# Kernel optimization log

Hardware: AMD Instinct MI355X
Metric: run time of the kernel (lower is better)

Reference implementation:

```python
import jax, jax.numpy as jnp
import numpy as np

B, T, D, H, L, V = 16, 1024, 512, 8, 6, 96
HS = D // H
FF = 4 * D


def setup_inputs() -> dict:
    key = jax.random.key(0)
    ks = jax.random.split(key, 16)
    n = lambda k, shape: jax.random.normal(k, shape, jnp.float32) * 0.02
    return {
        "idx": jax.random.randint(ks[0], (B, T), 0, V),
        "targets": jax.random.randint(ks[1], (B, T), 0, V),
        "tok_emb": n(ks[2], (V, D)),
        "pos_emb": n(ks[3], (T, D)),
        "Wq": n(ks[4], (L, H, D, HS)),
        "Wk": n(ks[5], (L, H, D, HS)),
        "Wv": n(ks[6], (L, H, D, HS)),
        "Wproj": n(ks[7], (L, D, D)),
        "bproj": jnp.zeros((L, D), jnp.float32),
        "W1": n(ks[8], (L, D, FF)),
        "b1": jnp.zeros((L, FF), jnp.float32),
        "W2": n(ks[9], (L, FF, D)),
        "b2": jnp.zeros((L, D), jnp.float32),
        "ln1_s": jnp.ones((L, D), jnp.float32),
        "ln1_b": jnp.zeros((L, D), jnp.float32),
        "ln2_s": jnp.ones((L, D), jnp.float32),
        "ln2_b": jnp.zeros((L, D), jnp.float32),
        "lnf_s": jnp.ones((D,), jnp.float32),
        "lnf_b": jnp.zeros((D,), jnp.float32),
        "Wout": n(ks[10], (D, V)),
        "bout": jnp.zeros((V,), jnp.float32),
    }


def _ln(x, s, b, eps=1e-5):
    m = x.mean(-1, keepdims=True)
    v = ((x - m) ** 2).mean(-1, keepdims=True)
    return (x - m) * jax.lax.rsqrt(v + eps) * s + b


def reference(idx, targets, tok_emb, pos_emb, Wq, Wk, Wv, Wproj, bproj,
              W1, b1, W2, b2, ln1_s, ln1_b, ln2_s, ln2_b, lnf_s, lnf_b,
              Wout, bout):
    x = tok_emb[idx] + pos_emb[:T]  # [B,T,D]
    causal = jnp.tril(jnp.ones((T, T), jnp.bool_))
    scale = D ** (-0.5)  # NOTE: source scales by full channel dim, not head_size
    for l in range(L):
        h = _ln(x, ln1_s[l], ln1_b[l])
        q = jnp.einsum("btd,hdk->bhtk", h, Wq[l])
        k = jnp.einsum("btd,hdk->bhtk", h, Wk[l])
        v = jnp.einsum("btd,hdk->bhtk", h, Wv[l])
        att = jnp.einsum("bhtk,bhsk->bhts", q, k) * scale
        att = jnp.where(causal, att, -jnp.inf)
        att = jax.nn.softmax(att, axis=-1)
        o = jnp.einsum("bhts,bhsk->bhtk", att, v)
        o = o.transpose(0, 2, 1, 3).reshape(B, T, D)  # concat heads
        x = x + (o @ Wproj[l] + bproj[l])
        h2 = _ln(x, ln2_s[l], ln2_b[l])
        x = x + (jnp.maximum(h2 @ W1[l] + b1[l], 0.0) @ W2[l] + b2[l])
    x = _ln(x, lnf_s, lnf_b)
    logits = (x @ Wout + bout).reshape(B * T, V)
    logp = jax.nn.log_softmax(logits, axis=-1)
    loss = -logp[jnp.arange(B * T), targets.reshape(-1)].mean()
    return logits, loss
```

## Files before the change

kernel.cpp:

```cpp
#include <hip/hip_runtime.h>

#define B_  16
#define T_  1024
#define D_  512
#define H_  8
#define L_  6
#define V_  96
#define HS_ 64
#define FF_ 2048
#define BT_ (B_*T_)
#define QKS 1024

typedef __attribute__((ext_vector_type(8))) short bf16x8;
typedef __attribute__((ext_vector_type(4))) float f32x4;

typedef __attribute__((address_space(3))) unsigned int lds_u32_t;
typedef const __attribute__((address_space(1))) unsigned int glb_u32_t;

__device__ __forceinline__ void gload16(const unsigned short* g, unsigned short* l) {
  __builtin_amdgcn_global_load_lds((glb_u32_t*)g, (lds_u32_t*)l, 16, 0, 0);
}

__device__ __forceinline__ unsigned short f2b(float f) {
  unsigned u = __float_as_uint(f);
  unsigned r = (u + 0x7FFFu + ((u >> 16) & 1u)) >> 16;
  return (unsigned short)r;
}

__global__ void zero_kernel(float* p) { p[0] = 0.f; }

__global__ __launch_bounds__(128) void embed_kernel(const int* __restrict__ idx,
    const float* __restrict__ tok, const float* __restrict__ pos, float* __restrict__ x) {
  int bt = blockIdx.x;
  int t  = bt & (T_ - 1);
  int id = idx[bt];
  if (id < 0) id = 0; if (id > V_ - 1) id = V_ - 1;
  int d  = threadIdx.x * 4;
  float4 tv = *(const float4*)(tok + (size_t)id * D_ + d);
  float4 pv = *(const float4*)(pos + (size_t)t  * D_ + d);
  float4 o = {tv.x + pv.x, tv.y + pv.y, tv.z + pv.z, tv.w + pv.w};
  *(float4*)(x + (size_t)bt * D_ + d) = o;
}

__global__ __launch_bounds__(256) void transpose_cvt(const float* __restrict__ src,
    unsigned short* __restrict__ dst, int R, int C, long sstride, long dstride,
    int zper, long zouter) {
  __shared__ float t[32][33];
  const float* s = src + (size_t)blockIdx.z * sstride;
  unsigned short* d = dst + (size_t)(blockIdx.z / zper) * zouter
                          + (size_t)(blockIdx.z % zper) * dstride;
  int r0 = blockIdx.y * 32, c0 = blockIdx.x * 32;
  int tr = threadIdx.x >> 5, tc = threadIdx.x & 31;
#pragma unroll
  for (int i = 0; i < 4; ++i)
    t[tr + i * 8][tc] = s[(size_t)(r0 + tr + i * 8) * C + c0 + tc];
  __syncthreads();
#pragma unroll
  for (int i = 0; i < 4; ++i)
    d[(size_t)(c0 + tr + i * 8) * R + r0 + tc] = f2b(t[tc][tr + i * 8]);
}

template<bool BF16OUT>
__global__ __launch_bounds__(256) void ln_kernel(const float* __restrict__ x,
    const float* __restrict__ s, const float* __restrict__ b, void* __restrict__ outv) {
  int wave = threadIdx.x >> 6;
  int lane = threadIdx.x & 63;
  int r = blockIdx.x * 4 + wave;
  const float* xr = x + (size_t)r * D_;
  float vals[8];
  float sum = 0.f;
#pragma unroll
  for (int j = 0; j < 8; ++j) { vals[j] = xr[j * 64 + lane]; sum += vals[j]; }
#pragma unroll
  for (int o = 32; o > 0; o >>= 1) sum += __shfl_xor(sum, o, 64);
  float mean = sum * (1.f / D_);
  float vs = 0.f;
#pragma unroll
  for (int j = 0; j < 8; ++j) { float d = vals[j] - mean; vs += d * d; }
#pragma unroll
  for (int o = 32; o > 0; o >>= 1) vs += __shfl_xor(vs, o, 64);
  float rstd = rsqrtf(vs * (1.f / D_) + 1e-5f);
#pragma unroll
  for (int j = 0; j < 8; ++j) {
    int c = j * 64 + lane;
    float v = (vals[j] - mean) * rstd * s[c] + b[c];
    if (BF16OUT) ((unsigned short*)outv)[(size_t)r * D_ + c] = f2b(v);
    else         ((float*)outv)[(size_t)r * D_ + c] = v;
  }
}

#define BK 32
template<bool ACC, bool RELU, bool BIAS, int OUTMODE, int MT, int NT>
__global__ __launch_bounds__(256) void mfma_gemm(
    const unsigned short* __restrict__ A,
    const unsigned short* __restrict__ Bt,
    const float* __restrict__ bias,
    void* __restrict__ Cv, void* __restrict__ Cv2,
    int K, int ldc) {
  constexpr int NI = (MT == 128) ? 4 : (NT == 128 ? 2 : 1);
  constexpr int WN = (MT == 128) ? 64 : (NT == 128 ? 32 : 16);
  __shared__ unsigned short Al[2][MT * BK];
  __shared__ unsigned short Bl[2][NT * BK];
  const int nwg = gridDim.x * gridDim.y;
  const int flat = blockIdx.x + gridDim.x * blockIdx.y;
  const int swz = (flat & 7) * (nwg >> 3) + (flat >> 3);
  const int bx = swz / gridDim.y;
  const int by = swz % gridDim.y;
  const int m0 = bx * MT, n0 = by * NT;
  const int tid = threadIdx.x;
  const int lane = tid & 63, wave = tid >> 6;
  const int wy = (MT == 128) ? (wave >> 1) : 0;
  const int wx = (MT == 128) ? (wave & 1) : wave;
  const int l15 = lane & 15, quad = lane >> 4;

  const int sbase = wave * 1024;
  const int soff  = sbase + lane * 16;
  const int r0 = soff >> 6, c0e = (soff & 63) >> 1;
  const int r1 = r0 + 64;
  const int ls = sbase >> 1;
  const unsigned short* gA0 = A  + (size_t)(m0 + r0) * K + c0e;
  const unsigned short* gA1 = A  + (size_t)(m0 + r1) * K + c0e;
  const unsigned short* gB0 = Bt + (size_t)(n0 + r0) * K + c0e;
  const unsigned short* gB1 = Bt + (size_t)(n0 + r1) * K + c0e;

  auto stage = [&](int buf, int k0) {
    gload16(gA0 + k0, &Al[buf][ls]);
    if constexpr (MT == 128) gload16(gA1 + k0, &Al[buf][ls + 2048]);
    gload16(gB0 + k0, &Bl[buf][ls]);
    if constexpr (NT == 128) gload16(gB1 + k0, &Bl[buf][ls + 2048]);
  };

  f32x4 acc[4][NI];
  const f32x4 z4 = {0.f, 0.f, 0.f, 0.f};
#pragma unroll
  for (int mi = 0; mi < 4; ++mi)
#pragma unroll
    for (int ni = 0; ni < NI; ++ni) acc[mi][ni] = z4;

  stage(0, 0);
  __syncthreads();

  const int nsteps = K / BK;
  int cur = 0;
  for (int s = 0; s < nsteps; ++s) {
    if (s + 1 < nsteps) stage(cur ^ 1, (s + 1) * BK);
    bf16x8 af[4], bfr[NI];
#pragma unroll
    for (int mi = 0; mi < 4; ++mi)
      af[mi] = *(const bf16x8*)(&Al[cur][(wy * 64 + mi * 16 + l15) * BK + quad * 8]);
#pragma unroll
    for (int ni = 0; ni < NI; ++ni)
      bfr[ni] = *(const bf16x8*)(&Bl[cur][(wx * WN + ni * 16 + l15) * BK + quad * 8]);
#pragma unroll
    for (int mi = 0; mi < 4; ++mi)
#pragma unroll
      for (int ni = 0; ni < NI; ++ni)
        acc[mi][ni] = __builtin_amdgcn_mfma_f32_16x16x32_bf16(af[mi], bfr[ni], acc[mi][ni], 0, 0, 0);
    if (s + 1 < nsteps) {
      __syncthreads();
      cur ^= 1;
    }
  }

#pragma unroll
  for (int mi = 0; mi < 4; ++mi) {
    int row0 = m0 + wy * 64 + mi * 16 + quad * 4;
#pragma unroll
    for (int ni = 0; ni < NI; ++ni) {
      int col = n0 + wx * WN + ni * 16 + l15;
      float bb = BIAS ? bias[col] : 0.f;
#pragma unroll
      for (int r = 0; r < 4; ++r) {
        float v = acc[mi][ni][r] + bb;
        if (RELU) v = fmaxf(v, 0.f);
        int row = row0 + r;
        if (OUTMODE == 3) {
          if (col < 1024) {
            ((unsigned short*)Cv)[(size_t)row * QKS + col] = f2b(v);
          } else {
            int vcol = col - 1024;
            int b = row >> 10, t = row & (T_ - 1);
            int h = vcol >> 6, hs = vcol & 63;
            ((unsigned short*)Cv2)[((size_t)((b * H_ + h) * HS_ + hs)) * T_ + t] = f2b(v);
          }
        } else {
          size_t off = (size_t)row * ldc + col;
          if (ACC) v += ((const float*)Cv)[off];
          if (OUTMODE == 1) ((unsigned short*)Cv)[off] = f2b(v);
          else              ((float*)Cv)[off] = v;
        }
      }
    }
  }
}

#define PSTR 72
__global__ __launch_bounds__(256) void attn_mfma(const unsigned short* __restrict__ q,
    const unsigned short* __restrict__ k, const unsigned short* __restrict__ vt,
    unsigned short* __restrict__ o) {
  __shared__ unsigned short Pbuf[2][64 * PSTR];
  __shared__ float Lsum[4][64];
  const int bh = blockIdx.y;
  const int b = bh >> 3, hh = bh & 7;
  const int tid = threadIdx.x;
  const int lane = tid & 63, w = tid >> 6;
  const int l15 = lane & 15, quad = lane >> 4;
  const float CEXP = 0.044194173824159216f * 1.4426950408889634f;

  const unsigned short* kbase = k  + (size_t)(b * T_ + w * 16 + l15) * QKS + hh * HS_ + quad * 8;
  const unsigned short* vbase = vt + ((size_t)(bh * HS_ + w * 16 + l15)) * T_ + quad * 8;
  const int gc = w * 16 + l15;
  const f32x4 z4 = {0.f, 0.f, 0.f, 0.f};

  for (int pass = 0; pass < 2; ++pass) {
    const int qt = pass ? (int)blockIdx.x : (T_ / 64 - 1 - (int)blockIdx.x);

    bf16x8 qf[4][2];
#pragma unroll
    for (int mi = 0; mi < 4; ++mi)
#pragma unroll
      for (int c = 0; c < 2; ++c)
        qf[mi][c] = *(const bf16x8*)(q + (size_t)(b * T_ + qt * 64 + mi * 16 + l15) * QKS
                                       + hh * HS_ + c * 32 + quad * 8);

    f32x4 oacc[4];
    float psum[4][4];
#pragma unroll
    for (int mi = 0; mi < 4; ++mi) {
      oacc[mi] = z4;
#pragma unroll
      for (int r = 0; r < 4; ++r) psum[mi][r] = 0.f;
    }

    bf16x8 kf[2], vf[2];
#pragma unroll
    for (int c = 0; c < 2; ++c) {
      kf[c] = *(const bf16x8*)(kbase + c * 32);
      vf[c] = *(const bf16x8*)(vbase + c * 32);
    }

    for (int kt = 0; kt <= qt; ++kt) {
      const int ktn = (kt < qt) ? kt + 1 : qt;
      bf16x8 kfn[2], vfn[2];
#pragma unroll
      for (int c = 0; c < 2; ++c) {
        kfn[c] = *(const bf16x8*)(kbase + (size_t)ktn * 64 * QKS + c * 32);
        vfn[c] = *(const bf16x8*)(vbase + ktn * 64 + c * 32);
      }

      f32x4 s[4];
#pragma unroll
      for (int mi = 0; mi < 4; ++mi) s[mi] = z4;
      __builtin_amdgcn_s_setprio(1);
#pragma unroll
      for (int c = 0; c < 2; ++c)
#pragma unroll
        for (int mi = 0; mi < 4; ++mi)
          s[mi] = __builtin_amdgcn_mfma_f32_16x16x32_bf16(qf[mi][c], kf[c], s[mi], 0, 0, 0);
      __builtin_amdgcn_s_setprio(0);

      unsigned short* pb = Pbuf[kt & 1];
      const bool diag = (kt == qt);
#pragma unroll
      for (int mi = 0; mi < 4; ++mi) {
        const int row0 = mi * 16 + quad * 4;
        float pv_[4];
#pragma unroll
        for (int r = 0; r < 4; ++r) {
          float p = exp2f(s[mi][r] * CEXP);
          if (diag && gc > row0 + r) p = 0.f;
          psum[mi][r] += p;
          pv_[r] = p;
        }
        unsigned pk01, pk23;
        asm("v_cvt_pk_bf16_f32 %0, %1, %2" : "=v"(pk01) : "v"(pv_[0]), "v"(pv_[1]));
        asm("v_cvt_pk_bf16_f32 %0, %1, %2" : "=v"(pk23) : "v"(pv_[2]), "v"(pv_[3]));
        const int base = row0 * PSTR + gc;
        pb[base]            = (unsigned short)(pk01 & 0xFFFFu);
        pb[base + PSTR]     = (unsigned short)(pk01 >> 16);
        pb[base + 2 * PSTR] = (unsigned short)(pk23 & 0xFFFFu);
        pb[base + 3 * PSTR] = (unsigned short)(pk23 >> 16);
      }
      __syncthreads();
      __builtin_amdgcn_s_setprio(1);
#pragma unroll
      for (int c = 0; c < 2; ++c) {
#pragma unroll
        for (int mi = 0; mi < 4; ++mi) {
          bf16x8 pf = *(const bf16x8*)(&pb[(mi * 16 + l15) * PSTR + c * 32 + quad * 8]);
          oacc[mi] = __builtin_amdgcn_mfma_f32_16x16x32_bf16(pf, vf[c], oacc[mi], 0, 0, 0);
        }
      }
      __builtin_amdgcn_s_setprio(0);
#pragma unroll
      for (int c = 0; c < 2; ++c) { kf[c] = kfn[c]; vf[c] = vfn[c]; }
    }

#pragma unroll
    for (int mi = 0; mi < 4; ++mi)
#pragma unroll
      for (int r = 0; r < 4; ++r) {
#pragma unroll
        for (int off = 1; off < 16; off <<= 1)
          psum[mi][r] += __shfl_xor(psum[mi][r], off, 64);
      }
    if (l15 == 0) {
#pragma unroll
      for (int mi = 0; mi < 4; ++mi)
#pragma unroll
        for (int r = 0; r < 4; ++r)
          Lsum[w][mi * 16 + quad * 4 + r] = psum[mi][r];
    }
    __syncthreads();
#pragma unroll
    for (int mi = 0; mi < 4; ++mi)
#pragma unroll
      for (int r = 0; r < 4; ++r) {
        int row = mi * 16 + quad * 4 + r;
        float inv = 1.f / (Lsum[0][row] + Lsum[1][row] + Lsum[2][row] + Lsum[3][row]);
        o[(size_t)(b * T_ + qt * 64 + row) * D_ + hh * HS_ + w * 16 + l15] =
            f2b(oacc[mi][r] * inv);
      }
  }
}

__global__ __launch_bounds__(256) void gemm_f32_kernel(const float* __restrict__ A, int lda,
    const float* __restrict__ Bw, int ldb, const float* __restrict__ bias,
    float* __restrict__ C, int ldc, int K, int N) {
  __shared__ float As[16][64];
  __shared__ float Bs[16][64];
  int n0 = blockIdx.y * 64;
  int nv = N - n0; if (nv > 64) nv = 64;
  int m0 = blockIdx.x * 64;
  const int tid = threadIdx.x;
  const int tx = tid & 15, ty = tid >> 4;
  const int amm = tid >> 2;
  const int akk = (tid & 3) * 4;
  const int bkk = tid >> 4;
  const int bnn = (tid & 15) * 4;
  float acc[4][4] = {};
  for (int k0 = 0; k0 < K; k0 += 16) {
    float4 av = *(const float4*)(A + (size_t)(m0 + amm) * lda + k0 + akk);
    As[akk + 0][amm] = av.x; As[akk + 1][amm] = av.y;
    As[akk + 2][amm] = av.z; As[akk + 3][amm] = av.w;
    if (bnn < nv) {
      float4 bv = *(const float4*)(Bw + (size_t)(k0 + bkk) * ldb + n0 + bnn);
      Bs[bkk][bnn + 0] = bv.x; Bs[bkk][bnn + 1] = bv.y;
      Bs[bkk][bnn + 2] = bv.z; Bs[bkk][bnn + 3] = bv.w;
    } else {
      Bs[bkk][bnn + 0] = 0.f; Bs[bkk][bnn + 1] = 0.f;
      Bs[bkk][bnn + 2] = 0.f; Bs[bkk][bnn + 3] = 0.f;
    }
    __syncthreads();
#pragma unroll
    for (int kk = 0; kk < 16; ++kk) {
      float4 a4 = *(const float4*)(&As[kk][ty * 4]);
      float4 b4 = *(const float4*)(&Bs[kk][tx * 4]);
      float aa[4] = {a4.x, a4.y, a4.z, a4.w};
      float bb[4] = {b4.x, b4.y, b4.z, b4.w};
#pragma unroll
      for (int i = 0; i < 4; ++i)
#pragma unroll
        for (int j = 0; j < 4; ++j)
          acc[i][j] = fmaf(aa[i], bb[j], acc[i][j]);
    }
    __syncthreads();
  }
  if (tx * 4 < nv) {
#pragma unroll
    for (int i = 0; i < 4; ++i) {
      float* cp = C + (size_t)(m0 + ty * 4 + i) * ldc + n0 + tx * 4;
      float4 st = {acc[i][0] + bias[n0 + tx * 4 + 0], acc[i][1] + bias[n0 + tx * 4 + 1],
                   acc[i][2] + bias[n0 + tx * 4 + 2], acc[i][3] + bias[n0 + tx * 4 + 3]};
      *(float4*)cp = st;
    }
  }
}

__global__ __launch_bounds__(256) void loss_kernel(const float* __restrict__ logits,
    const int* __restrict__ targets, float* __restrict__ loss_acc) {
  __shared__ float wsum[4];
  int wave = threadIdx.x >> 6, lane = threadIdx.x & 63;
  float local = 0.f;
  for (int r = blockIdx.x * 4 + wave; r < BT_; r += gridDim.x * 4) {
    const float* lr = logits + (size_t)r * V_;
    float v0 = lr[lane];
    float v1 = (lane < 32) ? lr[64 + lane] : -INFINITY;
    float mx = fmaxf(v0, v1);
#pragma unroll
    for (int o = 32; o > 0; o >>= 1) mx = fmaxf(mx, __shfl_xor(mx, o, 64));
    float se = expf(v0 - mx) + ((lane < 32) ? expf(v1 - mx) : 0.f);
#pragma unroll
    for (int o = 32; o > 0; o >>= 1) se += __shfl_xor(se, o, 64);
    if (lane == 0) {
      int tg = targets[r];
      if (tg < 0) tg = 0; if (tg > V_ - 1) tg = V_ - 1;
      local += (mx + logf(se)) - lr[tg];
    }
  }
  if (lane == 0) wsum[wave] = local;
  __syncthreads();
  if (threadIdx.x == 0)
    atomicAdd(loss_acc, wsum[0] + wsum[1] + wsum[2] + wsum[3]);
}

__global__ void loss_finalize_kernel(const float* __restrict__ acc, float* __restrict__ out) {
  out[(size_t)BT_ * V_] = acc[0] * (1.f / BT_);
}

static void* g_ws_fallback = nullptr;

extern "C" void kernel_launch(void* const* d_in, const int* in_sizes, int n_in,
                              void* d_out, int out_size, void* d_ws, size_t ws_size,
                              hipStream_t stream) {
  const int*   idx     = (const int*)d_in[0];
  const int*   targets = (const int*)d_in[1];
  const float* tok  = (const float*)d_in[2];
  const float* pos  = (const float*)d_in[3];
  const float* Wq   = (const float*)d_in[4];
  const float* Wk   = (const float*)d_in[5];
  const float* Wv   = (const float*)d_in[6];
  const float* Wp   = (const float*)d_in[7];
  const float* bp   = (const float*)d_in[8];
  const float* W1   = (const float*)d_in[9];
  const float* b1   = (const float*)d_in[10];
  const float* W2   = (const float*)d_in[11];
  const float* b2   = (const float*)d_in[12];
  const float* l1s  = (const float*)d_in[13];
  const float* l1b  = (const float*)d_in[14];
  const float* l2s  = (const float*)d_in[15];
  const float* l2b  = (const float*)d_in[16];
  const float* lfs  = (const float*)d_in[17];
  const float* lfb  = (const float*)d_in[18];
  const float* Wout = (const float*)d_in[19];
  const float* bout = (const float*)d_in[20];
  float* out = (float*)d_out;

  const size_t n_x  = (size_t)BT_ * D_;
  const size_t n_wT = 9437184;
  const size_t need_floats = n_x + n_x + n_x / 2 + n_x / 2 + n_x / 2 +
                             (size_t)BT_ * FF_ / 2 + n_wT + 256;
  const size_t need_bytes  = need_floats * sizeof(float);

  float* ws;
  if (ws_size >= need_bytes) {
    ws = (float*)d_ws;
  } else {
    if (!g_ws_fallback) (void)hipMalloc(&g_ws_fallback, need_bytes);
    ws = (float*)g_ws_fallback;
  }

  size_t off = 0;
  float* x  = ws + off; off += n_x;
  float* qf32 = ws + off; off += n_x;
  unsigned short* qkb = (unsigned short*)qf32;
  unsigned short* spare = (unsigned short*)(ws + off); off += n_x / 2;
  unsigned short* vtb = (unsigned short*)(ws + off); off += n_x / 2;
  unsigned short* hb  = (unsigned short*)(ws + off); off += n_x / 2;
  unsigned short* ffb = (unsigned short*)(ws + off); off += (size_t)BT_ * FF_ / 2;
  unsigned short* wqkvT = (unsigned short*)(ws + off);
  unsigned short* wpT = wqkvT + (size_t)L_ * 3 * D_ * D_;
  unsigned short* w1T = wpT + (size_t)L_ * D_ * D_;
  unsigned short* w2T = w1T + (size_t)L_ * D_ * FF_;
  off += n_wT;
  float* lacc = ws + off;
  (void)spare;

  const long DD = (long)D_ * D_;
  const long L3DD = 3 * DD;

  zero_kernel<<<1, 1, 0, stream>>>(lacc);
  embed_kernel<<<BT_, 128, 0, stream>>>(idx, tok, pos, x);

  transpose_cvt<<<dim3(2, 16, 48), 256, 0, stream>>>(Wq, wqkvT,            512, 64, 32768, 32768, 8, L3DD);
  transpose_cvt<<<dim3(2, 16, 48), 256, 0, stream>>>(Wk, wqkvT + DD,       512, 64, 32768, 32768, 8, L3DD);
  transpose_cvt<<<dim3(2, 16, 48), 256, 0, stream>>>(Wv, wqkvT + 2 * DD,   512, 64, 32768, 32768, 8, L3DD);
  transpose_cvt<<<dim3(16, 16, 6), 256, 0, stream>>>(Wp, wpT, 512, 512, 262144, 0, 1, 262144);
  transpose_cvt<<<dim3(64, 16, 6), 256, 0, stream>>>(W1, w1T, 512, 2048, 1048576, 0, 1, 1048576);
  transpose_cvt<<<dim3(16, 64, 6), 256, 0, stream>>>(W2, w2T, 2048, 512, 1048576, 0, 1, 1048576);

  const dim3 gQKV(BT_ / 128, 12);
  const dim3 gD64(BT_ / 64, D_ / 64);
  const dim3 gF(BT_ / 128, FF_ / 128);

  for (int l = 0; l < L_; ++l) {
    ln_kernel<true><<<BT_ / 4, 256, 0, stream>>>(x, l1s + (size_t)l * D_, l1b + (size_t)l * D_, hb);
    mfma_gemm<false, false, false, 3, 128, 128><<<gQKV, 256, 0, stream>>>(
        hb, wqkvT + (size_t)l * L3DD, nullptr, qkb, vtb, D_, 0);
    attn_mfma<<<dim3(T_ / 128, B_ * H_), 256, 0, stream>>>(qkb, qkb + 512, vtb, hb);
    mfma_gemm<true, false, true, 0, 64, 64><<<gD64, 256, 0, stream>>>(
        hb, wpT + (size_t)l * DD, bp + (size_t)l * D_, x, nullptr, D_, D_);
    ln_kernel<true><<<BT_ / 4, 256, 0, stream>>>(x, l2s + (size_t)l * D_, l2b + (size_t)l * D_, hb);
    mfma_gemm<false, true, true, 1, 128, 128><<<gF, 256, 0, stream>>>(
        hb, w1T + (size_t)l * D_ * FF_, b1 + (size_t)l * FF_, ffb, nullptr, D_, FF_);
    mfma_gemm<true, false, true, 0, 64, 64><<<gD64, 256, 0, stream>>>(
        ffb, w2T + (size_t)l * FF_ * D_, b2 + (size_t)l * D_, x, nullptr, FF_, D_);
  }

  ln_kernel<false><<<BT_ / 4, 256, 0, stream>>>(x, lfs, lfb, qf32);
  gemm_f32_kernel<<<dim3(BT_ / 64, 2), 256, 0, stream>>>(
      qf32, D_, Wout, V_, bout, out, V_, D_, V_);
  loss_kernel<<<1024, 256, 0, stream>>>(out, targets, lacc);
  loss_finalize_kernel<<<1, 1, 0, stream>>>(lacc, out);
}
```

Measured before the change: 1.961 ms.

## Add 256x256-tile 512-thread GEMM for QKV and FF1, widen residual GEMM tiles

Adds a new GEMM kernel with 256x256 output tiles, 8 waves, double-buffered LDS filled by direct global-to-LDS loads, XOR-swizzled LDS addressing, workgroup index swizzling and raised wave priority around the MFMA blocks. The QKV and FF1 projections switch to it to raise arithmetic intensity and cut global reloads of A and B. The residual projection GEMMs move from 64x64 to 64x128 tiles. The trade-off is fewer workgroups (384 for QKV, 512 for FF1) and higher register and LDS pressure, which may leave CUs underfilled.

Measured after the change: 1.832 ms. 1.07x faster.

```diff
diff --git a/kernel.cpp b/kernel.cpp
--- a/kernel.cpp
+++ b/kernel.cpp
@@ -188,6 +188,148 @@
           if (ACC) v += ((const float*)Cv)[off];
           if (OUTMODE == 1) ((unsigned short*)Cv)[off] = f2b(v);
           else              ((float*)Cv)[off] = v;
+        }
+      }
+    }
+  }
+}
+
+template<bool RELU, bool BIAS, int OUTMODE>
+__global__ __launch_bounds__(512) void mfma_gemm256(
+    const unsigned short* __restrict__ A,
+    const unsigned short* __restrict__ Bt,
+    const float* __restrict__ bias,
+    void* __restrict__ Cv, void* __restrict__ Cv2,
+    int K, int ldc) {
+  __shared__ unsigned short Al[2][2][8192];
+  __shared__ unsigned short Bl[2][2][8192];
+  const int nwg = gridDim.x * gridDim.y;
+  const int flat = blockIdx.x + gridDim.x * blockIdx.y;
+  const int swzb = (flat & 7) * (nwg >> 3) + (flat >> 3);
+  const int bx = swzb / gridDim.y, by = swzb % gridDim.y;
+  const int m0 = bx * 256, n0 = by * 256;
+  const int tid = threadIdx.x;
+  const int lane = tid & 63, w = tid >> 6;
+  const int wy = w >> 2, wx = w & 3;
+  const int l15 = lane & 15, quad = lane >> 4;
+
+  const int srow = w * 8 + (lane >> 3);
+  const int scol = (((lane & 7) * 16) ^ ((lane >> 5) << 5)) >> 1;
+  const int sb0 = w * 512;
+  const int sb1 = 4096 + w * 512;
+
+  const unsigned short* gA[2][2];
+  const unsigned short* gB[2][2];
+#pragma unroll
+  for (int h = 0; h < 2; ++h)
+#pragma unroll
+    for (int c = 0; c < 2; ++c) {
+      gA[h][c] = A  + (size_t)(m0 + h * 128 + c * 64 + srow) * K + scol;
+      gB[h][c] = Bt + (size_t)(n0 + h * 128 + c * 64 + srow) * K + scol;
+    }
+
+  f32x4 acc[8][4];
+  const f32x4 z4 = {0.f, 0.f, 0.f, 0.f};
+#pragma unroll
+  for (int mi = 0; mi < 8; ++mi)
+#pragma unroll
+    for (int ni = 0; ni < 4; ++ni) acc[mi][ni] = z4;
+
+#pragma unroll
+  for (int h = 0; h < 2; ++h) {
+    gload16(gA[h][0], &Al[0][h][sb0]);
+    gload16(gA[h][1], &Al[0][h][sb1]);
+    gload16(gB[h][0], &Bl[0][h][sb0]);
+    gload16(gB[h][1], &Bl[0][h][sb1]);
+  }
+  asm volatile("s_waitcnt vmcnt(0)" ::: "memory");
+  __builtin_amdgcn_s_barrier();
+  __builtin_amdgcn_sched_barrier(0);
+
+  const int NTt = K >> 6;
+  for (int t = 0; t < NTt; ++t) {
+    const int db = t & 1;
+    const int k1 = (t + 1) << 6;
+    const bool more = (t + 1 < NTt);
+    bf16x8 bfr[4][2];
+#pragma unroll
+    for (int q = 0; q < 4; ++q) {
+      bf16x8 af[2][2];
+#pragma unroll
+      for (int mm = 0; mm < 2; ++mm)
+#pragma unroll
+        for (int ks = 0; ks < 2; ++ks) {
+          int aoff = ((q * 2 + mm) * 16 + l15) * 128 + ks * 64 + quad * 16;
+          aoff ^= ((aoff >> 9) & 1) << 5;
+          af[mm][ks] = *(const bf16x8*)(&Al[db][wy][aoff >> 1]);
+        }
+      if (q == 0) {
+#pragma unroll
+        for (int n = 0; n < 4; ++n)
+#pragma unroll
+          for (int ks = 0; ks < 2; ++ks) {
+            int boff = ((wx & 1) * 64 + n * 16 + l15) * 128 + ks * 64 + quad * 16;
+            boff ^= ((boff >> 9) & 1) << 5;
+            bfr[n][ks] = *(const bf16x8*)(&Bl[db][wx >> 1][boff >> 1]);
+          }
+        if (more) {
+#pragma unroll
+          for (int h = 0; h < 2; ++h) {
+            gload16(gA[h][0] + k1, &Al[db ^ 1][h][sb0]);
+            gload16(gA[h][1] + k1, &Al[db ^ 1][h][sb1]);
+          }
+        }
+      } else if (q == 1) {
+        if (more) {
+#pragma unroll
+          for (int h = 0; h < 2; ++h) {
+            gload16(gB[h][0] + k1, &Bl[db ^ 1][h][sb0]);
+            gload16(gB[h][1] + k1, &Bl[db ^ 1][h][sb1]);
+          }
+        }
+      }
+      __builtin_amdgcn_s_setprio(1);
+#pragma unroll
+      for (int mm = 0; mm < 2; ++mm)
+#pragma unroll
+        for (int n = 0; n < 4; ++n)
+#pragma unroll
+          for (int ks = 0; ks < 2; ++ks)
+            acc[q * 2 + mm][n] = __builtin_amdgcn_mfma_f32_16x16x32_bf16(
+                af[mm][ks], bfr[n][ks], acc[q * 2 + mm][n], 0, 0, 0);
+      __builtin_amdgcn_s_setprio(0);
+      __builtin_amdgcn_sched_barrier(0);
+    }
+    if (more) {
+      asm volatile("s_waitcnt vmcnt(0)" ::: "memory");
+      __builtin_amdgcn_s_barrier();
+      __builtin_amdgcn_sched_barrier(0);
+    }
+  }
+
+#pragma unroll
+  for (int mi = 0; mi < 8; ++mi) {
+    int row0 = m0 + wy * 128 + mi * 16 + quad * 4;
+#pragma unroll
+    for (int ni = 0; ni < 4; ++ni) {
+      int col = n0 + wx * 64 + ni * 16 + l15;
+      float bb = BIAS ? bias[col] : 0.f;
+#pragma unroll
+      for (int r = 0; r < 4; ++r) {
+        float v = acc[mi][ni][r] + bb;
+        if (RELU) v = fmaxf(v, 0.f);
+        int row = row0 + r;
+        if (OUTMODE == 3) {
+          if (col < 1024) {
+            ((unsigned short*)Cv)[(size_t)row * QKS + col] = f2b(v);
+          } else {
+            int vcol = col - 1024;
+            int b = row >> 10, t = row & (T_ - 1);
+            int h = vcol >> 6, hs = vcol & 63;
+            ((unsigned short*)Cv2)[((size_t)((b * H_ + h) * HS_ + hs)) * T_ + t] = f2b(v);
+          }
+        } else {
+          ((unsigned short*)Cv)[(size_t)row * ldc + col] = f2b(v);
         }
       }
     }
@@ -479,21 +621,21 @@
   transpose_cvt<<<dim3(64, 16, 6), 256, 0, stream>>>(W1, w1T, 512, 2048, 1048576, 0, 1, 1048576);
   transpose_cvt<<<dim3(16, 64, 6), 256, 0, stream>>>(W2, w2T, 2048, 512, 1048576, 0, 1, 1048576);
 
-  const dim3 gQKV(BT_ / 128, 12);
-  const dim3 gD64(BT_ / 64, D_ / 64);
-  const dim3 gF(BT_ / 128, FF_ / 128);
+  const dim3 gQKV(BT_ / 256, 6);
+  const dim3 gFF1(BT_ / 256, FF_ / 256);
+  const dim3 gD64(BT_ / 64, D_ / 128);
 
   for (int l = 0; l < L_; ++l) {
     ln_kernel<true><<<BT_ / 4, 256, 0, stream>>>(x, l1s + (size_t)l * D_, l1b + (size_t)l * D_, hb);
-    mfma_gemm<false, false, false, 3, 128, 128><<<gQKV, 256, 0, stream>>>(
+    mfma_gemm256<false, false, 3><<<gQKV, 512, 0, stream>>>(
         hb, wqkvT + (size_t)l * L3DD, nullptr, qkb, vtb, D_, 0);
     attn_mfma<<<dim3(T_ / 128, B_ * H_), 256, 0, stream>>>(qkb, qkb + 512, vtb, hb);
-    mfma_gemm<true, false, true, 0, 64, 64><<<gD64, 256, 0, stream>>>(
+    mfma_gemm<true, false, true, 0, 64, 128><<<gD64, 256, 0, stream>>>(
         hb, wpT + (size_t)l * DD, bp + (size_t)l * D_, x, nullptr, D_, D_);
     ln_kernel<true><<<BT_ / 4, 256, 0, stream>>>(x, l2s + (size_t)l * D_, l2b + (size_t)l * D_, hb);
-    mfma_gemm<false, true, true, 1, 128, 128><<<gF, 256, 0, stream>>>(
+    mfma_gemm256<true, true, 1><<<gFF1, 512, 0, stream>>>(
         hb, w1T + (size_t)l * D_ * FF_, b1 + (size_t)l * FF_, ffb, nullptr, D_, FF_);
-    mfma_gemm<true, false, true, 0, 64, 64><<<gD64, 256, 0, stream>>>(
+    mfma_gemm<true, false, true, 0, 64, 128><<<gD64, 256, 0, stream>>>(
         ffb, w2T + (size_t)l * FF_ * D_, b2 + (size_t)l * D_, x, nullptr, FF_, D_);
   }
 
```
